# Performance work log

Measured on AMD Instinct MI355X. Metric: run time of the kernel, lower is better.

## Reference

```python
import jax, jax.numpy as jnp
import numpy as np

B, N, T, F, K = 32, 24, 12, 3, 3
COUT = 12                      # must equal T (LayerNorm applied to last dim = T)
DIN = N * COUT + N + 1         # 313 = lstm_in_dim
H = DIN * T                    # 3756 = lstm_hidden_dim (forced by residual add)
ODIM = 1
LN_EPS = 1e-5


def setup_inputs() -> dict:
    key = jax.random.key(0)
    ks = jax.random.split(key, 24)
    r = lambda i, shape, s=0.1: jax.random.normal(ks[i], shape, dtype=jnp.float32) * s
    return {
        "X": r(0, (B, N, T, F), 1.0),
        "cheb": r(1, (K, N, N), 0.3),
        # Spatial_Attention_layer (ASTGCN-style) params
        "sa_W1": r(2, (T,)), "sa_W2": r(3, (F, T)), "sa_W3": r(4, (F,)),
        "sa_bs": r(5, (1, N, N)), "sa_Vs": r(6, (N, N)),
        # Temporal_Attention_layer params
        "ta_U1": r(7, (N,)), "ta_U2": r(8, (F, N)), "ta_U3": r(9, (F,)),
        "ta_be": r(10, (1, T, T)), "ta_Ve": r(11, (T, T)),
        # ChebConv_with_sa params
        "theta": r(12, (K, F, COUT)), "cheb_bias": jnp.zeros((COUT,), jnp.float32),
        # LayerNorm
        "ln_g": jnp.ones((COUT,), jnp.float32), "ln_b": jnp.zeros((COUT,), jnp.float32),
        # layer_in: Linear(seq_len, seq_len)
        "layer_in_w": r(13, (T, T)), "layer_in_b": r(14, (T,)),
        # S_A2: Linear(lstm_in_dim, lstm_in_dim)
        "sa2_w": r(15, (DIN, DIN), 0.05), "sa2_b": r(16, (DIN,)),
        # LSTMCell (torch gate order i,f,g,o)
        "W_ih": r(17, (4 * H, DIN), 0.02), "W_hh": r(18, (4 * H, H), 0.01),
        "b_ih": jnp.zeros((4 * H,), jnp.float32), "b_hh": jnp.zeros((4 * H,), jnp.float32),
        # T_A2: Linear(seq_len*hidden, seq_len)
        "ta2_w": r(19, (T, T * H), 0.02), "ta2_b": r(20, (T,)),
        # layer_out
        "out_w": r(21, (ODIM, H), 0.02), "out_b": jnp.zeros((ODIM,), jnp.float32),
        # torch.randn initial states (fixed here for determinism)
        "h0": r(22, (B, H), 1.0), "c0": r(23, (B, H), 1.0),
    }


def reference(X, cheb, sa_W1, sa_W2, sa_W3, sa_bs, sa_Vs,
              ta_U1, ta_U2, ta_U3, ta_be, ta_Ve,
              theta, cheb_bias, ln_g, ln_b,
              layer_in_w, layer_in_b, sa2_w, sa2_b,
              W_ih, W_hh, b_ih, b_hh, ta2_w, ta2_b,
              out_w, out_b, h0, c0):
    sig = jax.nn.sigmoid
    Bsz = X.shape[0]
    x_flow = X[:, 0:1, :, 1]                     # (B,1,T)
    x_rain = X[:, :, :, 0]                       # (B,N,T)
    x_pre = jnp.concatenate([x_rain, x_flow], axis=1)  # (B,N+1,T)
    x4 = jnp.transpose(X, (0, 1, 3, 2))          # (B,N,F,T)

    # spatial attention; legacy nn.Softmax() on 3D tensor => axis=0
    lhs = jnp.einsum('bnf,ft->bnt', jnp.einsum('bnft,t->bnf', x4, sa_W1), sa_W2)
    rhs = jnp.einsum('f,bnft->btn', sa_W3, x4)
    S = jnp.einsum('nm,bmk->bnk', sa_Vs, sig(jnp.einsum('bnt,btm->bnm', lhs, rhs) + sa_bs))
    s_a = jax.nn.softmax(sig(jax.nn.softmax(S, axis=1)), axis=0)   # (B,N,N)

    # temporal attention
    xp = jnp.transpose(x4, (0, 3, 2, 1))         # (B,T,F,N)
    lhs_t = jnp.einsum('btf,fn->btn', jnp.einsum('btfn,n->btf', xp, ta_U1), ta_U2)
    rhs_t = jnp.einsum('f,bnft->bnt', ta_U3, x4)
    E = jnp.einsum('tu,buv->btv', ta_Ve, sig(jnp.einsum('btn,bnu->btu', lhs_t, rhs_t) + ta_be))
    t_a = jax.nn.softmax(sig(jax.nn.softmax(E, axis=1)), axis=0)   # (B,T,T)

    # attention-weighted Chebyshev conv; note reshape (not transpose), as in original
    xg = X.reshape(Bsz, N, F, -1)                # (B,N,F,T)
    Tk_at = cheb[None] * s_a[:, None]            # (B,K,N,N)
    rhs_g = jnp.einsum('bkmn,bmft->bknft', Tk_at, xg)
    xc = jax.nn.relu(jnp.einsum('bknft,kfo->bnot', rhs_g, theta) + cheb_bias[:, None])  # (B,N,COUT,T)

    # LayerNorm over last dim (T == COUT)
    mu = xc.mean(-1, keepdims=True)
    var = xc.var(-1, keepdims=True)
    x_ln = (xc - mu) / jnp.sqrt(var + LN_EPS) * ln_g + ln_b

    x_gc = x_ln.reshape(Bsz, -1, 12)             # (B, N*COUT, 12)
    x_gc_t = jnp.einsum('bij,bjk->bik', x_gc, t_a)
    x_res = jnp.concatenate([x_gc_t, x_pre], axis=1)   # (B, DIN, 12)
    x_in = x_res @ layer_in_w.T + layer_in_b     # Linear over last (seq) dim
    xs = jnp.transpose(x_in, (2, 0, 1))          # (T, B, DIN)

    def step(carry, x_t):
        h, c = carry
        alpha = jax.nn.softmax(sig(x_t @ sa2_w.T + sa2_b), axis=1)
        xi = x_t * alpha + x_t
        gates = xi @ W_ih.T + b_ih + h @ W_hh.T + b_hh
        i, f, g, o = jnp.split(gates, 4, axis=1)
        c2 = sig(f) * c + sig(i) * jnp.tanh(g)
        h2 = sig(o) * jnp.tanh(c2)
        return (h2, c2), h2

    _, hs = jax.lax.scan(step, (h0, c0), xs)     # (T,B,H)
    total_ht = jnp.transpose(hs, (1, 0, 2)).reshape(Bsz, -1)  # cat along dim 1, time-major
    beta = jax.nn.softmax(jax.nn.relu(total_ht @ ta2_w.T + ta2_b), axis=1)  # (B,T)
    out = jnp.einsum('tbh,bt->bh', hs, beta)
    out = out + x_in.reshape(Bsz, -1)            # requires H == DIN*T
    out = jax.nn.relu(out) @ out_w.T + out_b
    return out, s_a
```

## Files before the change

### kernel.cpp

```cpp
#include <hip/hip_runtime.h>

#define BSZ 32
#define NN 24
#define TT 12
#define FF 3
#define KK 3
#define COUT 12
#define DIN 313
#define HID 3756
#define H4 15024
#define KP 3776
#define KPI 320
#define NTILES 470
#define NB 235
#define NCH 30

using short8 = __attribute__((ext_vector_type(8))) short;
using f32x4  = __attribute__((ext_vector_type(4))) float;

__device__ inline unsigned short f2bf(float f){
  union{float f; unsigned u;} v; v.f=f;
  unsigned u=v.u;
  return (unsigned short)((u + 0x7FFFu + ((u>>16)&1u))>>16);
}
__device__ inline f32x4 mfma16(short8 a, short8 b, f32x4 c){
  return __builtin_amdgcn_mfma_f32_16x16x32_bf16(a,b,c,0,0,0);
}
__device__ inline float sigm(float x){ return 1.f/(1.f+expf(-x)); }

__global__ void __launch_bounds__(256) k_convpack(const float* __restrict__ W,
    unsigned short* __restrict__ Wp){
  __shared__ unsigned short lds[64*136];
  const int bi=blockIdx.x, cz=blockIdx.y, tid=threadIdx.x;
  for(int cg=cz; cg<NCH; cg+=6){
    int ks0=cg*4;
    int nks=min(4,118-ks0);
    int nf4=nks*8;
    for(int q=tid;q<64*nf4;q+=256){
      int r=q/nf4, f4=q-r*nf4;
      int g=r>>4, lj=r&15;
      int jj=bi*16+lj; if(jj>=HID) jj=HID-1;
      const float* src=W+(long)(g*HID+jj)*HID;
      int k=ks0*32+f4*4;
      ushort4 o;
      if(k+3<HID){
        float4 v=*(const float4*)(src+k);
        o.x=f2bf(v.x); o.y=f2bf(v.y); o.z=f2bf(v.z); o.w=f2bf(v.w);
      } else {
        float vv[4];
        #pragma unroll
        for(int t2=0;t2<4;t2++){ int kk=k+t2; vv[t2]=(kk<HID)?src[kk]:0.f; }
        o.x=f2bf(vv[0]); o.y=f2bf(vv[1]); o.z=f2bf(vv[2]); o.w=f2bf(vv[3]);
      }
      *(ushort4*)(&lds[r*136+f4*4])=o;
    }
    __syncthreads();
    for(int idx=tid; idx<nks*4*64; idx+=256){
      int l=idx&63, g=(idx>>6)&3, kl=idx>>8;
      int lj=l&15, lk=l>>4;
      short8 v=*(short8*)(&lds[(g*16+lj)*136 + kl*32 + lk*8]);
      *(short8*)(Wp + (((long)(bi*118+ks0+kl)*4+g)*64 + l)*8) = v;
    }
    __syncthreads();
  }
}

__global__ void k_convh(const float* __restrict__ h0f,
    unsigned short* __restrict__ hb0, unsigned short* __restrict__ hb1){
  const int g4=KP>>2;
  const int total=BSZ*g4;
  for(int i=blockIdx.x*blockDim.x+threadIdx.x; i<total; i+=gridDim.x*blockDim.x){
    int gq=i%g4, r=i/g4;
    int k=gq*4;
    float vv[4];
    if(k+3<HID){
      float4 x=*(const float4*)(h0f+(long)r*HID+k);
      vv[0]=x.x; vv[1]=x.y; vv[2]=x.z; vv[3]=x.w;
    } else {
      #pragma unroll
      for(int q=0;q<4;q++){ int kk=k+q; vv[q]=(kk<HID)? h0f[(long)r*HID+kk] : 0.f; }
    }
    ushort4 o;
    o.x=f2bf(vv[0]); o.y=f2bf(vv[1]); o.z=f2bf(vv[2]); o.w=f2bf(vv[3]);
    *(ushort4*)(hb0+(long)r*KP+k)=o;
    *(ushort4*)(hb1+(long)r*KP+k)=o;
  }
}

__global__ void k_attn(const float* __restrict__ X, const float* __restrict__ sa_W1,
   const float* __restrict__ sa_W2, const float* __restrict__ sa_W3,
   const float* __restrict__ sa_bs, const float* __restrict__ sa_Vs,
   const float* __restrict__ ta_U1, const float* __restrict__ ta_U2,
   const float* __restrict__ ta_U3, const float* __restrict__ ta_be,
   const float* __restrict__ ta_Ve,
   float* __restrict__ SA_pre, float* __restrict__ TA_pre){
  int b=blockIdx.x, tid=threadIdx.x;
  __shared__ float lin[864];
  __shared__ float lhs[NN*TT];
  __shared__ float rhs[TT*NN];
  __shared__ float P[NN*NN];
  __shared__ float S[NN*NN];
  __shared__ float lhsT[TT*NN];
  __shared__ float rhsT[NN*TT];
  __shared__ float PT[TT*TT];
  __shared__ float E[TT*TT];
  for(int i=tid;i<864;i+=256) lin[i]=X[b*864+i];
  __syncthreads();
  for(int i=tid;i<NN*TT;i+=256){ int n=i/TT, t=i%TT;
    float acc=0;
    #pragma unroll
    for(int f=0;f<FF;f++){
      float t1=0;
      for(int u=0;u<TT;u++) t1 += lin[n*36+u*3+f]*sa_W1[u];
      acc += t1*sa_W2[f*TT+t];
    }
    lhs[n*TT+t]=acc;
    float r=0;
    #pragma unroll
    for(int f=0;f<FF;f++) r += sa_W3[f]*lin[n*36+t*3+f];
    rhs[t*NN+n]=r;
  }
  for(int i=tid;i<TT*NN;i+=256){ int t=i/NN, n=i%NN;
    float acc=0;
    #pragma unroll
    for(int f=0;f<FF;f++){
      float t1=0;
      for(int m=0;m<NN;m++) t1 += lin[m*36+t*3+f]*ta_U1[m];
      acc += t1*ta_U2[f*NN+n];
    }
    lhsT[t*NN+n]=acc;
    float r=0;
    #pragma unroll
    for(int f=0;f<FF;f++) r += ta_U3[f]*lin[n*36+t*3+f];
    rhsT[n*TT+t]=r;
  }
  __syncthreads();
  for(int i=tid;i<NN*NN;i+=256){ int n=i/NN,m=i%NN;
    float a=0;
    for(int t=0;t<TT;t++) a+=lhs[n*TT+t]*rhs[t*NN+m];
    P[i]=sigm(a+sa_bs[i]);
  }
  for(int i=tid;i<TT*TT;i+=256){ int t=i/TT,u=i%TT;
    float a=0;
    for(int n=0;n<NN;n++) a+=lhsT[t*NN+n]*rhsT[n*TT+u];
    PT[i]=sigm(a+ta_be[i]);
  }
  __syncthreads();
  for(int i=tid;i<NN*NN;i+=256){ int n=i/NN,k=i%NN;
    float a=0;
    for(int m=0;m<NN;m++) a+=sa_Vs[n*NN+m]*P[m*NN+k];
    S[i]=a;
  }
  for(int i=tid;i<TT*TT;i+=256){ int t=i/TT,v=i%TT;
    float a=0;
    for(int u=0;u<TT;u++) a+=ta_Ve[t*TT+u]*PT[u*TT+v];
    E[i]=a;
  }
  __syncthreads();
  if(tid<NN){ int k=tid;
    float mx=-1e30f;
    for(int n=0;n<NN;n++) mx=fmaxf(mx,S[n*NN+k]);
    float sm=0;
    for(int n=0;n<NN;n++) sm+=__expf(S[n*NN+k]-mx);
    for(int n=0;n<NN;n++){
      float v=__expf(S[n*NN+k]-mx)/sm;
      SA_pre[b*576+n*NN+k]=sigm(v);
    }
  }
  if(tid>=32 && tid<32+TT){ int v=tid-32;
    float mx=-1e30f;
    for(int t=0;t<TT;t++) mx=fmaxf(mx,E[t*TT+v]);
    float sm=0;
    for(int t=0;t<TT;t++) sm+=__expf(E[t*TT+v]-mx);
    for(int t=0;t<TT;t++){
      float e=__expf(E[t*TT+v]-mx)/sm;
      TA_pre[b*144+t*TT+v]=sigm(e);
    }
  }
}

__global__ void k_bsoftmax(const float* __restrict__ SA_pre, const float* __restrict__ TA_pre,
    float* __restrict__ s_a, float* __restrict__ t_a, float* __restrict__ out_sa){
  int i=blockIdx.x*blockDim.x+threadIdx.x;
  if(i<576){
    float mx=-1e30f;
    for(int b=0;b<BSZ;b++) mx=fmaxf(mx,SA_pre[b*576+i]);
    float sm=0;
    for(int b=0;b<BSZ;b++) sm+=__expf(SA_pre[b*576+i]-mx);
    for(int b=0;b<BSZ;b++){
      float v=__expf(SA_pre[b*576+i]-mx)/sm;
      s_a[b*576+i]=v;
      out_sa[b*576+i]=v;
    }
  } else if(i<720){
    int j=i-576;
    float mx=-1e30f;
    for(int b=0;b<BSZ;b++) mx=fmaxf(mx,TA_pre[b*144+j]);
    float sm=0;
    for(int b=0;b<BSZ;b++) sm+=__expf(TA_pre[b*144+j]-mx);
    for(int b=0;b<BSZ;b++) t_a[b*144+j]=__expf(TA_pre[b*144+j]-mx)/sm;
  }
}

__global__ void k_graph(const float* __restrict__ X, const float* __restrict__ cheb,
  const float* __restrict__ s_a, const float* __restrict__ t_a,
  const float* __restrict__ theta, const float* __restrict__ cheb_bias,
  const float* __restrict__ ln_g, const float* __restrict__ ln_b,
  const float* __restrict__ liw, const float* __restrict__ lib,
  float* __restrict__ x_in){
  int b=blockIdx.x, tid=threadIdx.x;
  __shared__ float lin[864];
  __shared__ float A2[KK*NN*NN];
  __shared__ float rg[KK*NN*FF*TT];
  __shared__ float xc[NN*COUT*TT];
  __shared__ float xres[DIN*TT];
  __shared__ float ta_s[TT*TT];
  for(int i=tid;i<864;i+=320) lin[i]=X[b*864+i];
  for(int i=tid;i<KK*NN*NN;i+=320){ int mn=i%576; A2[i]=cheb[i]*s_a[b*576+mn]; }
  for(int i=tid;i<144;i+=320) ta_s[i]=t_a[b*144+i];
  __syncthreads();
  for(int i=tid;i<KK*NN*FF*TT;i+=320){
    int t=i%TT, f=(i/TT)%FF, n=(i/36)%NN, k=i/864;
    float a=0;
    for(int m=0;m<NN;m++) a+=A2[k*576+m*NN+n]*lin[m*36+f*TT+t];
    rg[i]=a;
  }
  __syncthreads();
  for(int i=tid;i<NN*COUT*TT;i+=320){
    int t=i%TT, o=(i/TT)%COUT, n=i/(COUT*TT);
    float a=cheb_bias[o];
    #pragma unroll
    for(int k=0;k<KK;k++)
      #pragma unroll
      for(int f=0;f<FF;f++)
        a += rg[((k*NN+n)*FF+f)*TT+t]*theta[(k*FF+f)*COUT+o];
    xc[i]=fmaxf(a,0.f);
  }
  __syncthreads();
  if(tid<NN*COUT){
    float mu=0;
    for(int t=0;t<TT;t++) mu+=xc[tid*TT+t];
    mu*=(1.f/12.f);
    float var=0;
    for(int t=0;t<TT;t++){ float d=xc[tid*TT+t]-mu; var+=d*d; }
    var*=(1.f/12.f);
    float inv=rsqrtf(var+1e-5f);
    for(int t=0;t<TT;t++) xc[tid*TT+t]=(xc[tid*TT+t]-mu)*inv*ln_g[t]+ln_b[t];
  }
  __syncthreads();
  for(int i=tid;i<NN*COUT;i+=320){
    for(int v=0;v<TT;v++){
      float a=0;
      for(int t=0;t<TT;t++) a+=xc[i*TT+t]*ta_s[t*TT+v];
      xres[i*TT+v]=a;
    }
  }
  for(int i=tid;i<25*TT;i+=320){
    int r=i/TT, t=i%TT;
    float v=(r<NN)? lin[r*36+t*3+0] : lin[t*3+1];
    xres[(288+r)*TT+t]=v;
  }
  __syncthreads();
  for(int i=tid;i<DIN;i+=320){
    for(int t=0;t<TT;t++){
      float a=lib[t];
      #pragma unroll
      for(int u=0;u<TT;u++) a+=xres[i*TT+u]*liw[t*TT+u];
      x_in[((long)b*DIN+i)*TT+t]=a;
    }
  }
}

__global__ void __launch_bounds__(512) k_alpha(const float* __restrict__ x_in,
    const float* __restrict__ sa2_w, const float* __restrict__ sa2_b,
    unsigned short* __restrict__ xi_b){
  int blk=blockIdx.x; int t=blk>>5, b=blk&31; int tid=threadIdx.x;
  __shared__ float xt[DIN];
  __shared__ float red[512];
  if(tid<DIN) xt[tid]=x_in[((long)b*DIN+tid)*TT+t];
  __syncthreads();
  float z=-1e30f, e=0.f;
  if(tid<DIN){
    float a=sa2_b[tid];
    const float* wr=sa2_w+(long)tid*DIN;
    for(int i=0;i<DIN;i++) a+=xt[i]*wr[i];
    z=sigm(a);
  }
  red[tid]=z; __syncthreads();
  for(int off=256;off>0;off>>=1){ if(tid<off) red[tid]=fmaxf(red[tid],red[tid+off]); __syncthreads(); }
  float mx=red[0]; __syncthreads();
  e=(tid<DIN)?__expf(z-mx):0.f;
  red[tid]=e; __syncthreads();
  for(int off=256;off>0;off>>=1){ if(tid<off) red[tid]+=red[tid+off]; __syncthreads(); }
  float sm=red[0];
  if(tid<KPI){
    unsigned short v=0;
    if(tid<DIN){
      float alpha=e/sm;
      v=f2bf(xt[tid]*alpha+xt[tid]);
    }
    xi_b[(long)blk*KPI+tid]=v;
  }
}

__global__ void __launch_bounds__(256) k_gx(const unsigned short* __restrict__ xi,
   const float* __restrict__ Wih, const float* __restrict__ b_ih,
   const float* __restrict__ b_hh, float* __restrict__ Gx){
  int w=threadIdx.x>>6, lane=threadIdx.x&63;
  int jt=blockIdx.x*4+w;
  if(jt>=NTILES) return;
  int j0=jt*32;
  int lj=lane&15, lk=lane>>4;
  short8 bfr[10][2];
  #pragma unroll
  for(int ks=0;ks<10;ks++)
    #pragma unroll
    for(int jh=0;jh<2;jh++){
      int j=j0+jh*16+lj;
      short8 bv;
      #pragma unroll
      for(int q=0;q<8;q++){
        int k=ks*32+lk*8+q;
        float f=(j<H4 && k<DIN)? Wih[(long)j*DIN+k] : 0.f;
        bv[q]=(short)f2bf(f);
      }
      bfr[ks][jh]=bv;
    }
  for(int t=0;t<TT;t++){
    f32x4 acc[2][2]={};
    #pragma unroll
    for(int ks=0;ks<10;ks++){
      #pragma unroll
      for(int mh=0;mh<2;mh++){
        short8 a=*(const short8*)(xi + ((long)(t*32+mh*16+lj))*KPI + ks*32 + lk*8);
        acc[mh][0]=mfma16(a,bfr[ks][0],acc[mh][0]);
        acc[mh][1]=mfma16(a,bfr[ks][1],acc[mh][1]);
      }
    }
    #pragma unroll
    for(int mh=0;mh<2;mh++)
      #pragma unroll
      for(int jh=0;jh<2;jh++){
        int j=j0+jh*16+lj;
        if(j<H4){
          float bias=b_ih[j]+b_hh[j];
          #pragma unroll
          for(int r=0;r<4;r++){
            int bb=mh*16+lk*4+r;
            Gx[((long)t*32+bb)*H4+j]=acc[mh][jh][r]+bias;
          }
        }
      }
  }
}

__global__ void __launch_bounds__(512) k_step(const unsigned short* __restrict__ hb_r,
    unsigned short* __restrict__ hb_w, const unsigned short* __restrict__ Wp,
    const float* __restrict__ Gx, const float* __restrict__ c0,
    float* __restrict__ c, float* __restrict__ hs, int t){
  const int tid=threadIdx.x;
  const int w=tid>>6, lane=tid&63;
  const int j0=blockIdx.x*16;
  const int lj=lane&15, lk=lane>>4;
  const int s0=(118*w)>>3, s1=(118*(w+1))>>3;
  const unsigned short* slab = Wp + (long)blockIdx.x*64*KP;
  f32x4 acc[4][2]={};
  #pragma unroll 2
  for(int ks=s0;ks<s1;ks++){
    int kofs=ks*32+lk*8;
    short8 a0=*(const short8*)(hb_r + (long)lj*KP + kofs);
    short8 a1=*(const short8*)(hb_r + (long)(16+lj)*KP + kofs);
    const unsigned short* pk = slab + ((long)ks<<11);
    #pragma unroll
    for(int g=0;g<4;g++){
      short8 bv=*(const short8*)(pk + (g<<9) + (lane<<3));
      acc[g][0]=mfma16(a0,bv,acc[g][0]);
      acc[g][1]=mfma16(a1,bv,acc[g][1]);
    }
  }
  __shared__ float red[8][4][512];
  #pragma unroll
  for(int g=0;g<4;g++)
    #pragma unroll
    for(int mh=0;mh<2;mh++)
      #pragma unroll
      for(int r=0;r<4;r++)
        red[w][g][(mh*16+lk*4+r)*16+lj]=acc[g][mh][r];
  __syncthreads();
  if(tid<512){
    int p=tid;
    int bb=p>>4, jl=p&15; int j=j0+jl;
    if(j<HID){
      long gxo=((long)t*BSZ+bb)*H4 + j;
      float si=0,sf=0,sg=0,so=0;
      #pragma unroll
      for(int ww=0;ww<8;ww++){
        si+=red[ww][0][p]; sf+=red[ww][1][p];
        sg+=red[ww][2][p]; so+=red[ww][3][p];
      }
      si+=Gx[gxo]; sf+=Gx[gxo+HID]; sg+=Gx[gxo+2*HID]; so+=Gx[gxo+3*HID];
      float gi=sigm(si), gf=sigm(sf), gg=tanhf(sg), go=sigm(so);
      int idx=bb*HID+j;
      float cin=(t==0)?c0[idx]:c[idx];
      float c2=gf*cin+gi*gg;
      float h2=go*tanhf(c2);
      c[idx]=c2;
      hs[(long)t*BSZ*HID+idx]=h2;
      hb_w[(long)bb*KP+j]=f2bf(h2);
    }
  }
}

__global__ void k_tail(const float* __restrict__ hs, const float* __restrict__ ta2_w,
   const float* __restrict__ ta2_b, const float* __restrict__ x_in,
   const float* __restrict__ out_w, const float* __restrict__ out_b,
   float* __restrict__ out0){
  int b=blockIdx.x, tid=threadIdx.x;
  float p[12]={0,0,0,0,0,0,0,0,0,0,0,0};
  for(int idx=tid; idx<TT*HID; idx+=256){
    int t=idx/HID, j=idx-t*HID;
    float v=hs[((long)t*BSZ+b)*HID+j];
    #pragma unroll
    for(int q=0;q<12;q++) p[q]+=v*ta2_w[(long)q*TT*HID+idx];
  }
  __shared__ float red[256];
  __shared__ float bt[12];
  float z[12];
  #pragma unroll
  for(int q=0;q<12;q++){
    __syncthreads();
    red[tid]=p[q]; __syncthreads();
    for(int off=128;off>0;off>>=1){ if(tid<off) red[tid]+=red[tid+off]; __syncthreads(); }
    z[q]=red[0];
  }
  if(tid==0){
    float mx=-1e30f;
    #pragma unroll
    for(int q=0;q<12;q++){ z[q]=fmaxf(z[q]+ta2_b[q],0.f); mx=fmaxf(mx,z[q]); }
    float sm=0;
    #pragma unroll
    for(int q=0;q<12;q++){ z[q]=__expf(z[q]-mx); sm+=z[q]; }
    #pragma unroll
    for(int q=0;q<12;q++) bt[q]=z[q]/sm;
  }
  __syncthreads();
  float acc=0;
  for(int j=tid;j<HID;j+=256){
    float ov=0;
    #pragma unroll
    for(int t=0;t<TT;t++) ov+=hs[((long)t*BSZ+b)*HID+j]*bt[t];
    ov+=x_in[(long)b*HID+j];
    acc+=fmaxf(ov,0.f)*out_w[j];
  }
  __syncthreads();
  red[tid]=acc; __syncthreads();
  for(int off=128;off>0;off>>=1){ if(tid<off) red[tid]+=red[tid+off]; __syncthreads(); }
  if(tid==0) out0[b]=red[0]+out_b[0];
}

extern "C" void kernel_launch(void* const* d_in, const int* in_sizes, int n_in,
                              void* d_out, int out_size, void* d_ws, size_t ws_size,
                              hipStream_t stream){
  (void)in_sizes; (void)n_in; (void)out_size; (void)ws_size;
  const float* X     =(const float*)d_in[0];
  const float* cheb  =(const float*)d_in[1];
  const float* sa_W1 =(const float*)d_in[2];
  const float* sa_W2 =(const float*)d_in[3];
  const float* sa_W3 =(const float*)d_in[4];
  const float* sa_bs =(const float*)d_in[5];
  const float* sa_Vs =(const float*)d_in[6];
  const float* ta_U1 =(const float*)d_in[7];
  const float* ta_U2 =(const float*)d_in[8];
  const float* ta_U3 =(const float*)d_in[9];
  const float* ta_be =(const float*)d_in[10];
  const float* ta_Ve =(const float*)d_in[11];
  const float* theta =(const float*)d_in[12];
  const float* cb    =(const float*)d_in[13];
  const float* ln_g  =(const float*)d_in[14];
  const float* ln_b  =(const float*)d_in[15];
  const float* liw   =(const float*)d_in[16];
  const float* lib   =(const float*)d_in[17];
  const float* sa2_w =(const float*)d_in[18];
  const float* sa2_b =(const float*)d_in[19];
  const float* W_ih  =(const float*)d_in[20];
  const float* W_hh  =(const float*)d_in[21];
  const float* b_ih  =(const float*)d_in[22];
  const float* b_hh  =(const float*)d_in[23];
  const float* ta2_w =(const float*)d_in[24];
  const float* ta2_b =(const float*)d_in[25];
  const float* out_w =(const float*)d_in[26];
  const float* out_b =(const float*)d_in[27];
  const float* h0    =(const float*)d_in[28];
  const float* c0    =(const float*)d_in[29];

  char* w=(char*)d_ws;
  unsigned short* Wp =(unsigned short*)(w);
  float* Gx   =(float*)(w+113582080);
  float* hs   =(float*)(w+136658944);
  unsigned short* hb0=(unsigned short*)(w+142428160);
  unsigned short* hb1=(unsigned short*)(w+142669824);
  float* c    =(float*)(w+142911488);
  float* x_in =(float*)(w+143392256);
  unsigned short* xi_b=(unsigned short*)(w+143873024);
  float* SA   =(float*)(w+144118784);
  float* TA   =(float*)(w+144192512);
  float* s_a  =(float*)(w+144210944);
  float* t_a  =(float*)(w+144284672);
  float* out_f=(float*)d_out;

  k_convpack<<<dim3(NB,6),256,0,stream>>>(W_hh,Wp);
  k_convh<<<118,256,0,stream>>>(h0,hb0,hb1);
  k_attn<<<32,256,0,stream>>>(X,sa_W1,sa_W2,sa_W3,sa_bs,sa_Vs,ta_U1,ta_U2,ta_U3,ta_be,ta_Ve,SA,TA);
  k_bsoftmax<<<3,256,0,stream>>>(SA,TA,s_a,t_a,out_f+32);
  k_graph<<<32,320,0,stream>>>(X,cheb,s_a,t_a,theta,cb,ln_g,ln_b,liw,lib,x_in);
  k_alpha<<<384,512,0,stream>>>(x_in,sa2_w,sa2_b,xi_b);
  k_gx<<<118,256,0,stream>>>(xi_b,W_ih,b_ih,b_hh,Gx);
  unsigned short* hb[2]={hb0,hb1};
  for(int t=0;t<TT;t++)
    k_step<<<NB,512,0,stream>>>(hb[t&1],hb[(t+1)&1],Wp,Gx,c0,c,hs,t);
  k_tail<<<32,256,0,stream>>>(hs,ta2_w,ta2_b,x_in,out_w,out_b,out_f);
}
```

Before: 577.4 us.

## Spread W_hh bf16 packing across the small prologue kernels as extra blocks

Removes the standalone W_hh conversion/pack kernel and the h0 conversion kernel. Their work is split into chunk ranges handled by extra blocks appended to the attention, graph, alpha and input-gate kernels, so the large weight repack runs alongside those latency-bound, low-occupancy kernels. The batch softmax is also folded into the graph kernel: each block recomputes the column softmax it needs, which drops a launch and the s_a/t_a round trip. This cuts the launch count from seven to four, at the cost of redundant softmax work and more shared memory per block in the fused kernels.

New measurement: 577.8 us. No clear change (+0.1%).

```diff
diff --git a/kernel.cpp b/kernel.cpp
--- a/kernel.cpp
+++ b/kernel.cpp
@@ -28,15 +28,13 @@
 }
 __device__ inline float sigm(float x){ return 1.f/(1.f+expf(-x)); }
 
-__global__ void __launch_bounds__(256) k_convpack(const float* __restrict__ W,
-    unsigned short* __restrict__ Wp){
-  __shared__ unsigned short lds[64*136];
-  const int bi=blockIdx.x, cz=blockIdx.y, tid=threadIdx.x;
-  for(int cg=cz; cg<NCH; cg+=6){
+__device__ void conv_slab(const float* __restrict__ W, unsigned short* __restrict__ Wp,
+    int bi, int cg0, int cg1, int tid, int nthr, unsigned short* lds){
+  for(int cg=cg0; cg<cg1; cg++){
     int ks0=cg*4;
     int nks=min(4,118-ks0);
     int nf4=nks*8;
-    for(int q=tid;q<64*nf4;q+=256){
+    for(int q=tid;q<64*nf4;q+=nthr){
       int r=q/nf4, f4=q-r*nf4;
       int g=r>>4, lj=r&15;
       int jj=bi*16+lj; if(jj>=HID) jj=HID-1;
@@ -55,7 +53,7 @@
       *(ushort4*)(&lds[r*136+f4*4])=o;
     }
     __syncthreads();
-    for(int idx=tid; idx<nks*4*64; idx+=256){
+    for(int idx=tid; idx<nks*4*64; idx+=nthr){
       int l=idx&63, g=(idx>>6)&3, kl=idx>>8;
       int lj=l&15, lk=l>>4;
       short8 v=*(short8*)(&lds[(g*16+lj)*136 + kl*32 + lk*8]);
@@ -65,45 +63,24 @@
   }
 }
 
-__global__ void k_convh(const float* __restrict__ h0f,
-    unsigned short* __restrict__ hb0, unsigned short* __restrict__ hb1){
-  const int g4=KP>>2;
-  const int total=BSZ*g4;
-  for(int i=blockIdx.x*blockDim.x+threadIdx.x; i<total; i+=gridDim.x*blockDim.x){
-    int gq=i%g4, r=i/g4;
-    int k=gq*4;
-    float vv[4];
-    if(k+3<HID){
-      float4 x=*(const float4*)(h0f+(long)r*HID+k);
-      vv[0]=x.x; vv[1]=x.y; vv[2]=x.z; vv[3]=x.w;
-    } else {
-      #pragma unroll
-      for(int q=0;q<4;q++){ int kk=k+q; vv[q]=(kk<HID)? h0f[(long)r*HID+kk] : 0.f; }
-    }
-    ushort4 o;
-    o.x=f2bf(vv[0]); o.y=f2bf(vv[1]); o.z=f2bf(vv[2]); o.w=f2bf(vv[3]);
-    *(ushort4*)(hb0+(long)r*KP+k)=o;
-    *(ushort4*)(hb1+(long)r*KP+k)=o;
-  }
-}
-
-__global__ void k_attn(const float* __restrict__ X, const float* __restrict__ sa_W1,
-   const float* __restrict__ sa_W2, const float* __restrict__ sa_W3,
-   const float* __restrict__ sa_bs, const float* __restrict__ sa_Vs,
-   const float* __restrict__ ta_U1, const float* __restrict__ ta_U2,
-   const float* __restrict__ ta_U3, const float* __restrict__ ta_be,
-   const float* __restrict__ ta_Ve,
-   float* __restrict__ SA_pre, float* __restrict__ TA_pre){
-  int b=blockIdx.x, tid=threadIdx.x;
-  __shared__ float lin[864];
-  __shared__ float lhs[NN*TT];
-  __shared__ float rhs[TT*NN];
-  __shared__ float P[NN*NN];
-  __shared__ float S[NN*NN];
-  __shared__ float lhsT[TT*NN];
-  __shared__ float rhsT[NN*TT];
-  __shared__ float PT[TT*TT];
-  __shared__ float E[TT*TT];
+__global__ void __launch_bounds__(256) k_f1(const float* __restrict__ X,
+   const float* __restrict__ sa_W1, const float* __restrict__ sa_W2,
+   const float* __restrict__ sa_W3, const float* __restrict__ sa_bs,
+   const float* __restrict__ sa_Vs, const float* __restrict__ ta_U1,
+   const float* __restrict__ ta_U2, const float* __restrict__ ta_U3,
+   const float* __restrict__ ta_be, const float* __restrict__ ta_Ve,
+   float* __restrict__ SA_pre, float* __restrict__ TA_pre,
+   const float* __restrict__ W, unsigned short* __restrict__ Wp){
+  __shared__ __align__(16) float smf[4352];
+  int tid=threadIdx.x;
+  if(blockIdx.x>=32){
+    conv_slab(W,Wp,blockIdx.x-32,0,8,tid,256,(unsigned short*)smf);
+    return;
+  }
+  int b=blockIdx.x;
+  float* lin=smf;        float* lhs=smf+864;   float* rhs=smf+1152;
+  float* P=smf+1440;     float* S=smf+2016;    float* lhsT=smf+2592;
+  float* rhsT=smf+2880;  float* PT=smf+3168;   float* E=smf+3312;
   for(int i=tid;i<864;i+=256) lin[i]=X[b*864+i];
   __syncthreads();
   for(int i=tid;i<NN*TT;i+=256){ int n=i/TT, t=i%TT;
@@ -179,45 +156,47 @@
   }
 }
 
-__global__ void k_bsoftmax(const float* __restrict__ SA_pre, const float* __restrict__ TA_pre,
-    float* __restrict__ s_a, float* __restrict__ t_a, float* __restrict__ out_sa){
-  int i=blockIdx.x*blockDim.x+threadIdx.x;
-  if(i<576){
+__global__ void __launch_bounds__(320) k_f2(const float* __restrict__ X,
+  const float* __restrict__ cheb, const float* __restrict__ SA_pre,
+  const float* __restrict__ TA_pre, const float* __restrict__ theta,
+  const float* __restrict__ cheb_bias, const float* __restrict__ ln_g,
+  const float* __restrict__ ln_b, const float* __restrict__ liw,
+  const float* __restrict__ lib, float* __restrict__ x_in,
+  float* __restrict__ out_sa,
+  const float* __restrict__ W, unsigned short* __restrict__ Wp){
+  __shared__ __align__(16) float smf[13116];
+  int tid=threadIdx.x;
+  if(blockIdx.x>=32){
+    conv_slab(W,Wp,blockIdx.x-32,8,16,tid,320,(unsigned short*)smf);
+    return;
+  }
+  int b=blockIdx.x;
+  float* lin =smf;
+  float* A2  =smf+864;
+  float* rg  =smf+2592;
+  float* xc  =smf+5184;
+  float* xres=smf+8640;
+  float* tal =smf+12396;
+  float* sa_l=smf+12540;
+  for(int i=tid;i<864;i+=320) lin[i]=X[b*864+i];
+  for(int i=tid;i<576;i+=320){
     float mx=-1e30f;
-    for(int b=0;b<BSZ;b++) mx=fmaxf(mx,SA_pre[b*576+i]);
+    for(int bb=0;bb<BSZ;bb++) mx=fmaxf(mx,SA_pre[bb*576+i]);
     float sm=0;
-    for(int b=0;b<BSZ;b++) sm+=__expf(SA_pre[b*576+i]-mx);
-    for(int b=0;b<BSZ;b++){
-      float v=__expf(SA_pre[b*576+i]-mx)/sm;
-      s_a[b*576+i]=v;
-      out_sa[b*576+i]=v;
-    }
-  } else if(i<720){
-    int j=i-576;
+    for(int bb=0;bb<BSZ;bb++) sm+=__expf(SA_pre[bb*576+i]-mx);
+    float v=__expf(SA_pre[b*576+i]-mx)/sm;
+    sa_l[i]=v;
+    out_sa[b*576+i]=v;
+  }
+  for(int i=tid;i<144;i+=320){
     float mx=-1e30f;
-    for(int b=0;b<BSZ;b++) mx=fmaxf(mx,TA_pre[b*144+j]);
+    for(int bb=0;bb<BSZ;bb++) mx=fmaxf(mx,TA_pre[bb*144+i]);
     float sm=0;
-    for(int b=0;b<BSZ;b++) sm+=__expf(TA_pre[b*144+j]-mx);
-    for(int b=0;b<BSZ;b++) t_a[b*144+j]=__expf(TA_pre[b*144+j]-mx)/sm;
-  }
-}
-
-__global__ void k_graph(const float* __restrict__ X, const float* __restrict__ cheb,
-  const float* __restrict__ s_a, const float* __restrict__ t_a,
-  const float* __restrict__ theta, const float* __restrict__ cheb_bias,
-  const float* __restrict__ ln_g, const float* __restrict__ ln_b,
-  const float* __restrict__ liw, const float* __restrict__ lib,
-  float* __restrict__ x_in){
-  int b=blockIdx.x, tid=threadIdx.x;
-  __shared__ float lin[864];
-  __shared__ float A2[KK*NN*NN];
-  __shared__ float rg[KK*NN*FF*TT];
-  __shared__ float xc[NN*COUT*TT];
-  __shared__ float xres[DIN*TT];
-  __shared__ float ta_s[TT*TT];
-  for(int i=tid;i<864;i+=320) lin[i]=X[b*864+i];
-  for(int i=tid;i<KK*NN*NN;i+=320){ int mn=i%576; A2[i]=cheb[i]*s_a[b*576+mn]; }
-  for(int i=tid;i<144;i+=320) ta_s[i]=t_a[b*144+i];
+    for(int bb=0;bb<BSZ;bb++) sm+=__expf(TA_pre[bb*144+i]-mx);
+    tal[i]=__expf(TA_pre[b*144+i]-mx)/sm;
+  }
+  __syncthreads();
+  for(int i=tid;i<KK*NN*NN;i+=320){ int mn=i%576; A2[i]=cheb[i]*sa_l[mn]; }
   __syncthreads();
   for(int i=tid;i<KK*NN*FF*TT;i+=320){
     int t=i%TT, f=(i/TT)%FF, n=(i/36)%NN, k=i/864;
@@ -251,7 +230,7 @@
   for(int i=tid;i<NN*COUT;i+=320){
     for(int v=0;v<TT;v++){
       float a=0;
-      for(int t=0;t<TT;t++) a+=xc[i*TT+t]*ta_s[t*TT+v];
+      for(int t=0;t<TT;t++) a+=xc[i*TT+t]*tal[t*TT+v];
       xres[i*TT+v]=a;
     }
   }
@@ -271,12 +250,19 @@
   }
 }
 
-__global__ void __launch_bounds__(512) k_alpha(const float* __restrict__ x_in,
+__global__ void __launch_bounds__(512) k_f3(const float* __restrict__ x_in,
     const float* __restrict__ sa2_w, const float* __restrict__ sa2_b,
-    unsigned short* __restrict__ xi_b){
-  int blk=blockIdx.x; int t=blk>>5, b=blk&31; int tid=threadIdx.x;
-  __shared__ float xt[DIN];
-  __shared__ float red[512];
+    unsigned short* __restrict__ xi_b,
+    const float* __restrict__ W, unsigned short* __restrict__ Wp){
+  __shared__ __align__(16) float smf[4352];
+  int tid=threadIdx.x;
+  if(blockIdx.x>=384){
+    conv_slab(W,Wp,blockIdx.x-384,16,23,tid,512,(unsigned short*)smf);
+    return;
+  }
+  int blk=blockIdx.x; int t=blk>>5, b=blk&31;
+  float* xt=smf;
+  float* red=smf+320;
   if(tid<DIN) xt[tid]=x_in[((long)b*DIN+tid)*TT+t];
   __syncthreads();
   float z=-1e30f, e=0.f;
@@ -303,10 +289,37 @@
   }
 }
 
-__global__ void __launch_bounds__(256) k_gx(const unsigned short* __restrict__ xi,
+__global__ void __launch_bounds__(256) k_f4(const unsigned short* __restrict__ xi,
    const float* __restrict__ Wih, const float* __restrict__ b_ih,
-   const float* __restrict__ b_hh, float* __restrict__ Gx){
-  int w=threadIdx.x>>6, lane=threadIdx.x&63;
+   const float* __restrict__ b_hh, float* __restrict__ Gx,
+   const float* __restrict__ W, unsigned short* __restrict__ Wp,
+   const float* __restrict__ h0f, unsigned short* __restrict__ hb0,
+   unsigned short* __restrict__ hb1){
+  __shared__ __align__(16) float smf[4352];
+  int tid=threadIdx.x;
+  if(blockIdx.x>=118){
+    int cb_=blockIdx.x-118;
+    conv_slab(W,Wp,cb_,23,30,tid,256,(unsigned short*)smf);
+    const int g4=KP>>2;
+    for(int i=cb_*256+tid; i<BSZ*g4; i+=NB*256){
+      int gq=i%g4, r=i/g4;
+      int k=gq*4;
+      float vv[4];
+      if(k+3<HID){
+        float4 x=*(const float4*)(h0f+(long)r*HID+k);
+        vv[0]=x.x; vv[1]=x.y; vv[2]=x.z; vv[3]=x.w;
+      } else {
+        #pragma unroll
+        for(int q=0;q<4;q++){ int kk=k+q; vv[q]=(kk<HID)? h0f[(long)r*HID+kk] : 0.f; }
+      }
+      ushort4 o;
+      o.x=f2bf(vv[0]); o.y=f2bf(vv[1]); o.z=f2bf(vv[2]); o.w=f2bf(vv[3]);
+      *(ushort4*)(hb0+(long)r*KP+k)=o;
+      *(ushort4*)(hb1+(long)r*KP+k)=o;
+    }
+    return;
+  }
+  int w=tid>>6, lane=tid&63;
   int jt=blockIdx.x*4+w;
   if(jt>=NTILES) return;
   int j0=jt*32;
@@ -504,17 +517,13 @@
   unsigned short* xi_b=(unsigned short*)(w+143873024);
   float* SA   =(float*)(w+144118784);
   float* TA   =(float*)(w+144192512);
-  float* s_a  =(float*)(w+144210944);
-  float* t_a  =(float*)(w+144284672);
   float* out_f=(float*)d_out;
 
-  k_convpack<<<dim3(NB,6),256,0,stream>>>(W_hh,Wp);
-  k_convh<<<118,256,0,stream>>>(h0,hb0,hb1);
-  k_attn<<<32,256,0,stream>>>(X,sa_W1,sa_W2,sa_W3,sa_bs,sa_Vs,ta_U1,ta_U2,ta_U3,ta_be,ta_Ve,SA,TA);
-  k_bsoftmax<<<3,256,0,stream>>>(SA,TA,s_a,t_a,out_f+32);
-  k_graph<<<32,320,0,stream>>>(X,cheb,s_a,t_a,theta,cb,ln_g,ln_b,liw,lib,x_in);
-  k_alpha<<<384,512,0,stream>>>(x_in,sa2_w,sa2_b,xi_b);
-  k_gx<<<118,256,0,stream>>>(xi_b,W_ih,b_ih,b_hh,Gx);
+  k_f1<<<32+NB,256,0,stream>>>(X,sa_W1,sa_W2,sa_W3,sa_bs,sa_Vs,ta_U1,ta_U2,ta_U3,ta_be,ta_Ve,
+                               SA,TA,W_hh,Wp);
+  k_f2<<<32+NB,320,0,stream>>>(X,cheb,SA,TA,theta,cb,ln_g,ln_b,liw,lib,x_in,out_f+32,W_hh,Wp);
+  k_f3<<<384+NB,512,0,stream>>>(x_in,sa2_w,sa2_b,xi_b,W_hh,Wp);
+  k_f4<<<118+NB,256,0,stream>>>(xi_b,W_ih,b_ih,b_hh,Gx,W_hh,Wp,h0,hb0,hb1);
   unsigned short* hb[2]={hb0,hb1};
   for(int t=0;t<TT;t++)
     k_step<<<NB,512,0,stream>>>(hb[t&1],hb[(t+1)&1],Wp,Gx,c0,c,hs,t);
```
